# Kernel tuning notes

Hardware: AMD Instinct MI355X
Metric: run time of the kernel (lower is better)

Reference implementation:

```python
import jax, jax.numpy as jnp
import numpy as np

BLK = 128          # stk blocking
HID = 1024         # hidden_size
FFN = 4096         # ffn_hidden_size per expert
NE = 8             # moe_num_experts
TOK = 8192         # padded tokens (multiple of BLK)


def setup_inputs() -> dict:
    key = jax.random.key(0)
    k1, k2, k3 = jax.random.split(key, 3)
    x = jax.random.normal(k1, (TOK, HID), dtype=jnp.float32)
    w1 = jax.random.normal(k2, (NE * FFN, HID), dtype=jnp.float32) * 0.02
    n_row_blocks = TOK // BLK          # 64
    cols_per_expert = FFN // BLK       # 32
    # dMoE topology: each token row-block is assigned one expert; its nonzero
    # column blocks are all ffn blocks of that expert.
    expert_assign = jax.random.randint(k3, (n_row_blocks,), 0, NE)
    row_indices = jnp.repeat(jnp.arange(n_row_blocks), cols_per_expert)
    column_indices = (expert_assign[:, None] * cols_per_expert
                      + jnp.arange(cols_per_expert)[None, :]).reshape(-1)
    return {
        "x": x,
        "w1": w1,
        "row_indices": row_indices.astype(jnp.int32),     # [nnz]
        "column_indices": column_indices.astype(jnp.int32),  # [nnz]
        "block": BLK,
    }


def reference(x, w1, row_indices, column_indices, block):
    # sdd(x, w1.T, topo): out block k = x_block[row_indices[k]] @ w1_block[column_indices[k]].T
    hid = x.shape[1]
    xb = x.reshape(-1, block, hid)    # [n_row_blocks, blk, hid]
    wb = w1.reshape(-1, block, hid)   # [n_col_blocks, blk, hid]
    # [nnz, blk, blk] block-sparse data of the output matrix
    return jnp.einsum('kbh,kch->kbc', xb[row_indices], wb[column_indices])
```

## Files before the change

kernel.cpp:

```cpp
#include <hip/hip_runtime.h>
#include <hip/hip_bf16.h>
#include <stdint.h>

#define HID 1024
#define BLKDIM 128
#define BKT 32
#define NKT (HID / BKT)
#define NBUF 3

using short8 = __attribute__((ext_vector_type(8))) short;
using f32x4  = __attribute__((ext_vector_type(4))) float;
using f32x4v = __attribute__((ext_vector_type(4))) float;
using u32x4v = __attribute__((ext_vector_type(4))) unsigned int;

__device__ __forceinline__ uint32_t bfround(float f) {
    uint32_t u = __builtin_bit_cast(uint32_t, f);
    return (u + 0x7FFFu + ((u >> 16) & 1u)) >> 16;
}

__device__ __forceinline__ void gld16(const ushort* g, const ushort* lds_base) {
    __builtin_amdgcn_global_load_lds(
        (const __attribute__((address_space(1))) void*)g,
        (__attribute__((address_space(3))) void*)lds_base, 16, 0, 0);
}

__global__ __launch_bounds__(256)
void cvt_bf16_kernel(const float* __restrict__ src, uint4* __restrict__ dst, int n8) {
    int i = blockIdx.x * blockDim.x + threadIdx.x;
    if (i >= n8) return;
    const f32x4v* s = reinterpret_cast<const f32x4v*>(src) + (size_t)i * 2;
    f32x4v v0 = __builtin_nontemporal_load(s);
    f32x4v v1 = __builtin_nontemporal_load(s + 1);
    uint4 w;
    w.x = bfround(v0.x) | (bfround(v0.y) << 16);
    w.y = bfround(v0.z) | (bfround(v0.w) << 16);
    w.z = bfround(v1.x) | (bfround(v1.y) << 16);
    w.w = bfround(v1.z) | (bfround(v1.w) << 16);
    dst[i] = w;
}

__global__ __launch_bounds__(512, 4)
void sdd_pipe2_kernel(const ushort* __restrict__ xb, const ushort* __restrict__ wb,
                      const int* __restrict__ rind, const int* __restrict__ cind,
                      float* __restrict__ out) {
    __shared__ ushort sA[NBUF][BLKDIM * BKT];
    __shared__ ushort sB[NBUF][2 * BLKDIM * BKT];

    int g = blockIdx.x;
    const int nwg = gridDim.x;
    if ((nwg & 7) == 0) {
        const int cpx = nwg >> 3;
        g = (g & 7) * cpx + (g >> 3);
    }
    const int k0 = g * 2;
    const int r  = rind[k0];

    const int t = threadIdx.x;
    const int w = t >> 6;
    const int l = t & 63;

    const int unx   = (l & 7) ^ ((l >> 3) & 7);
    const int rin16 = 2 * (l >> 3) + (unx >> 2);
    const int kofs  = (unx & 3) * 8;

    const ushort* agb = xb + (size_t)(r * BLKDIM + w * 16 + rin16) * HID + kofs;
    const int cblk = cind[k0 + (w >> 2)];
    const ushort* bgb = wb + (size_t)(cblk * BLKDIM + (w & 3) * 32 + rin16) * HID + kofs;

    const int wr   = (w >> 2) * 64;
    const int wcol = (w & 3) * 64;
    const int ps_l = (((l >> 4) + ((l & 1) << 2)) ^ ((l & 15) >> 1)) * 8;
    const int rhalf = (l & 15) >> 1;

    int aoff[4], boff[4];
#pragma unroll
    for (int m = 0; m < 4; ++m) aoff[m] = (wr / 2 + m * 8 + rhalf) * 64 + ps_l;
#pragma unroll
    for (int n = 0; n < 4; ++n) boff[n] = (wcol / 2 + n * 8 + rhalf) * 64 + ps_l;

    f32x4 acc[4][4];
#pragma unroll
    for (int m = 0; m < 4; ++m)
#pragma unroll
        for (int n = 0; n < 4; ++n)
            acc[m][n] = (f32x4){0.f, 0.f, 0.f, 0.f};

    auto stage = [&](int b, int kt) {
        gld16(agb + kt * BKT, &sA[b][w * 512]);
        gld16(bgb + kt * BKT,                      &sB[b][(2 * w) * 512]);
        gld16(bgb + (size_t)16 * HID + kt * BKT,   &sB[b][(2 * w + 1) * 512]);
    };

    stage(0, 0);
    stage(1, 1);
    asm volatile("s_waitcnt vmcnt(3)" ::: "memory");
    __builtin_amdgcn_s_barrier();
    __builtin_amdgcn_sched_barrier(0);

    for (int kt = 0; kt < NKT; ++kt) {
        const int cur = kt % 3;
        const int nxt = (kt + 2) % 3;
        const bool pre = (kt + 2) < NKT;
        const ushort* sa = &sA[cur][0];
        const ushort* sb = &sB[cur][0];

        if (pre) stage(nxt, kt + 2);

        short8 aF[4], bF[4];
#pragma unroll
        for (int m = 0; m < 4; ++m)
            aF[m] = *reinterpret_cast<const short8*>(&sa[aoff[m]]);
#pragma unroll
        for (int n = 0; n < 4; ++n)
            bF[n] = *reinterpret_cast<const short8*>(&sb[boff[n]]);
        __builtin_amdgcn_s_setprio(1);
#pragma unroll
        for (int m = 0; m < 4; ++m)
#pragma unroll
            for (int n = 0; n < 4; ++n)
                acc[m][n] = __builtin_amdgcn_mfma_f32_16x16x32_bf16(aF[m], bF[n], acc[m][n], 0, 0, 0);
        __builtin_amdgcn_s_setprio(0);

        if (pre) asm volatile("s_waitcnt vmcnt(3)" ::: "memory");
        else     asm volatile("s_waitcnt vmcnt(0)" ::: "memory");
        __builtin_amdgcn_s_barrier();
        __builtin_amdgcn_sched_barrier(0);
    }

    const int blk = (w & 3) >> 1;
    float* op = out + (size_t)(k0 + blk) * (BLKDIM * BLKDIM);
    const int colbase = (wcol & 64) ? 64 : 0;
    const int lr = l & 15;
    const int rbase = wr + (l >> 4) * 4;
#pragma unroll
    for (int m = 0; m < 4; ++m)
#pragma unroll
        for (int n = 0; n < 4; ++n) {
            const int col = colbase + n * 16 + lr;
#pragma unroll
            for (int j = 0; j < 4; ++j)
                __builtin_nontemporal_store(acc[m][n][j],
                    &op[(size_t)(rbase + m * 16 + j) * BLKDIM + col]);
        }
}

__device__ __forceinline__ void store16f(ushort* dst, float4 v0, float4 v1, float4 v2, float4 v3) {
    uint4 w0, w1;
    w0.x = bfround(v0.x) | (bfround(v0.y) << 16);
    w0.y = bfround(v0.z) | (bfround(v0.w) << 16);
    w0.z = bfround(v1.x) | (bfround(v1.y) << 16);
    w0.w = bfround(v1.z) | (bfround(v1.w) << 16);
    w1.x = bfround(v2.x) | (bfround(v2.y) << 16);
    w1.y = bfround(v2.z) | (bfround(v2.w) << 16);
    w1.z = bfround(v3.x) | (bfround(v3.y) << 16);
    w1.w = bfround(v3.z) | (bfround(v3.w) << 16);
    uint4* d = reinterpret_cast<uint4*>(dst);
    d[0] = w0; d[1] = w1;
}

__global__ __launch_bounds__(256, 2)
void sdd_bf16_kernel(const float* __restrict__ x, const float* __restrict__ w1,
                     const int* __restrict__ rind, const int* __restrict__ cind,
                     float* __restrict__ out) {
    __shared__ ushort sA[2][BLKDIM * 32];
    __shared__ ushort sB[2][BLKDIM * 32];
    const int k = blockIdx.x;
    const int t = threadIdx.x;
    const int r = rind[k];
    const int c = cind[k];
    const float* Abase = x  + (size_t)r * BLKDIM * HID;
    const float* Bbase = w1 + (size_t)c * BLKDIM * HID;
    const int srow = t >> 1, shalf = t & 1;
    const float* aptr = Abase + (size_t)srow * HID + shalf * 16;
    const float* bptr = Bbase + (size_t)srow * HID + shalf * 16;
    const int soff = srow * 32 + shalf * 16;
    const int wv = t >> 6, lane = t & 63;
    const int wr = (wv >> 1) * 64, wc = (wv & 1) * 64;
    const int lr = lane & 15, lk = (lane >> 4) * 8;
    f32x4 acc[4][4];
#pragma unroll
    for (int m = 0; m < 4; ++m)
#pragma unroll
        for (int n = 0; n < 4; ++n) acc[m][n] = (f32x4){0.f, 0.f, 0.f, 0.f};
    float4 ra[4], rb[4];
#pragma unroll
    for (int i = 0; i < 4; ++i) {
        ra[i] = *reinterpret_cast<const float4*>(aptr + i * 4);
        rb[i] = *reinterpret_cast<const float4*>(bptr + i * 4);
    }
    store16f(&sA[0][soff], ra[0], ra[1], ra[2], ra[3]);
    store16f(&sB[0][soff], rb[0], rb[1], rb[2], rb[3]);
    __syncthreads();
    for (int kt = 0; kt < 32; ++kt) {
        const int cur = kt & 1;
        if (kt + 1 < 32) {
            const float* ap = aptr + (kt + 1) * 32;
            const float* bp = bptr + (kt + 1) * 32;
#pragma unroll
            for (int i = 0; i < 4; ++i) {
                ra[i] = *reinterpret_cast<const float4*>(ap + i * 4);
                rb[i] = *reinterpret_cast<const float4*>(bp + i * 4);
            }
        }
        const ushort* sa = sA[cur];
        const ushort* sb = sB[cur];
        short8 aF[4], bF[4];
#pragma unroll
        for (int m = 0; m < 4; ++m) aF[m] = *reinterpret_cast<const short8*>(&sa[(wr + m * 16 + lr) * 32 + lk]);
#pragma unroll
        for (int n = 0; n < 4; ++n) bF[n] = *reinterpret_cast<const short8*>(&sb[(wc + n * 16 + lr) * 32 + lk]);
#pragma unroll
        for (int m = 0; m < 4; ++m)
#pragma unroll
            for (int n = 0; n < 4; ++n)
                acc[m][n] = __builtin_amdgcn_mfma_f32_16x16x32_bf16(aF[m], bF[n], acc[m][n], 0, 0, 0);
        if (kt + 1 < 32) {
            store16f(&sA[cur ^ 1][soff], ra[0], ra[1], ra[2], ra[3]);
            store16f(&sB[cur ^ 1][soff], rb[0], rb[1], rb[2], rb[3]);
        }
        __syncthreads();
    }
    float* op = out + (size_t)k * (BLKDIM * BLKDIM);
    const int rbase = wr + (lane >> 4) * 4;
#pragma unroll
    for (int m = 0; m < 4; ++m)
#pragma unroll
        for (int n = 0; n < 4; ++n) {
            const int col = wc + n * 16 + lr;
#pragma unroll
            for (int j = 0; j < 4; ++j)
                op[(size_t)(rbase + m * 16 + j) * BLKDIM + col] = acc[m][n][j];
        }
}

extern "C" void kernel_launch(void* const* d_in, const int* in_sizes, int n_in,
                              void* d_out, int out_size, void* d_ws, size_t ws_size,
                              hipStream_t stream) {
    const float* x  = (const float*)d_in[0];
    const float* w1 = (const float*)d_in[1];
    const int* ri   = (const int*)d_in[2];
    const int* ci   = (const int*)d_in[3];
    float* out      = (float*)d_out;
    const int nnz   = in_sizes[2];
    const int nx    = in_sizes[0];
    const int nw    = in_sizes[1];

    const size_t need = ((size_t)nx + (size_t)nw) * sizeof(ushort);
    if (ws_size >= need && (nnz & 1) == 0) {
        ushort* xb = (ushort*)d_ws;
        ushort* wb = xb + nx;
        const int nx8 = nx / 8, nw8 = nw / 8;
        hipLaunchKernelGGL(cvt_bf16_kernel, dim3((nx8 + 255) / 256), dim3(256), 0, stream,
                           x, (uint4*)xb, nx8);
        hipLaunchKernelGGL(cvt_bf16_kernel, dim3((nw8 + 255) / 256), dim3(256), 0, stream,
                           w1, (uint4*)wb, nw8);
        hipLaunchKernelGGL(sdd_pipe2_kernel, dim3(nnz / 2), dim3(512), 0, stream,
                           xb, wb, ri, ci, out);
    } else {
        hipLaunchKernelGGL(sdd_bf16_kernel, dim3(nnz), dim3(256), 0, stream,
                           x, w1, ri, ci, out);
    }
}
```

Measured before the change: 148.8 us.

## Stage epilogue through LDS for vectorized 16-byte output stores and move prefetch after fragment loads

Result: faster. 141.2 us (-5.1%).

```diff
diff --git a/kernel.cpp b/kernel.cpp
--- a/kernel.cpp
+++ b/kernel.cpp
@@ -11,7 +11,6 @@
 using short8 = __attribute__((ext_vector_type(8))) short;
 using f32x4  = __attribute__((ext_vector_type(4))) float;
 using f32x4v = __attribute__((ext_vector_type(4))) float;
-using u32x4v = __attribute__((ext_vector_type(4))) unsigned int;
 
 __device__ __forceinline__ uint32_t bfround(float f) {
     uint32_t u = __builtin_bit_cast(uint32_t, f);
@@ -43,8 +42,7 @@
 void sdd_pipe2_kernel(const ushort* __restrict__ xb, const ushort* __restrict__ wb,
                       const int* __restrict__ rind, const int* __restrict__ cind,
                       float* __restrict__ out) {
-    __shared__ ushort sA[NBUF][BLKDIM * BKT];
-    __shared__ ushort sB[NBUF][2 * BLKDIM * BKT];
+    __shared__ ushort lds[NBUF * BLKDIM * BKT + NBUF * 2 * BLKDIM * BKT];
 
     int g = blockIdx.x;
     const int nwg = gridDim.x;
@@ -59,6 +57,9 @@
     const int w = t >> 6;
     const int l = t & 63;
 
+    ushort* sAb = lds;
+    ushort* sBb = lds + NBUF * BLKDIM * BKT;
+
     const int unx   = (l & 7) ^ ((l >> 3) & 7);
     const int rin16 = 2 * (l >> 3) + (unx >> 2);
     const int kofs  = (unx & 3) * 8;
@@ -86,9 +87,9 @@
             acc[m][n] = (f32x4){0.f, 0.f, 0.f, 0.f};
 
     auto stage = [&](int b, int kt) {
-        gld16(agb + kt * BKT, &sA[b][w * 512]);
-        gld16(bgb + kt * BKT,                      &sB[b][(2 * w) * 512]);
-        gld16(bgb + (size_t)16 * HID + kt * BKT,   &sB[b][(2 * w + 1) * 512]);
+        gld16(agb + kt * BKT, &sAb[b * 4096 + w * 512]);
+        gld16(bgb + kt * BKT,                      &sBb[b * 8192 + (2 * w) * 512]);
+        gld16(bgb + (size_t)16 * HID + kt * BKT,   &sBb[b * 8192 + (2 * w + 1) * 512]);
     };
 
     stage(0, 0);
@@ -101,10 +102,8 @@
         const int cur = kt % 3;
         const int nxt = (kt + 2) % 3;
         const bool pre = (kt + 2) < NKT;
-        const ushort* sa = &sA[cur][0];
-        const ushort* sb = &sB[cur][0];
-
-        if (pre) stage(nxt, kt + 2);
+        const ushort* sa = &sAb[cur * 4096];
+        const ushort* sb = &sBb[cur * 8192];
 
         short8 aF[4], bF[4];
 #pragma unroll
@@ -113,6 +112,7 @@
 #pragma unroll
         for (int n = 0; n < 4; ++n)
             bF[n] = *reinterpret_cast<const short8*>(&sb[boff[n]]);
+        if (pre) stage(nxt, kt + 2);
         __builtin_amdgcn_s_setprio(1);
 #pragma unroll
         for (int m = 0; m < 4; ++m)
@@ -130,18 +130,24 @@
     const int blk = (w & 3) >> 1;
     float* op = out + (size_t)(k0 + blk) * (BLKDIM * BLKDIM);
     const int colbase = (wcol & 64) ? 64 : 0;
-    const int lr = l & 15;
-    const int rbase = wr + (l >> 4) * 4;
-#pragma unroll
-    for (int m = 0; m < 4; ++m)
-#pragma unroll
-        for (int n = 0; n < 4; ++n) {
-            const int col = colbase + n * 16 + lr;
+    float* scr = reinterpret_cast<float*>(lds) + w * 1152;
+
+#pragma unroll
+    for (int m = 0; m < 4; ++m) {
+#pragma unroll
+        for (int n = 0; n < 4; ++n)
 #pragma unroll
             for (int j = 0; j < 4; ++j)
-                __builtin_nontemporal_store(acc[m][n][j],
-                    &op[(size_t)(rbase + m * 16 + j) * BLKDIM + col]);
-        }
+                scr[((l >> 4) * 4 + j) * 72 + n * 16 + (l & 15)] = acc[m][n][j];
+#pragma unroll
+        for (int rg = 0; rg < 4; ++rg) {
+            const int tr = rg * 4 + (l >> 4);
+            f32x4 v = *reinterpret_cast<const f32x4*>(&scr[tr * 72 + (l & 15) * 4]);
+            __builtin_nontemporal_store(v,
+                reinterpret_cast<f32x4*>(&op[(size_t)(wr + m * 16 + tr) * BLKDIM
+                                             + colbase + (l & 15) * 4]));
+        }
+    }
 }
 
 __device__ __forceinline__ void store16f(ushort* dst, float4 v0, float4 v1, float4 v2, float4 v3) {
```
